# Kernel optimization log

Measured on AMD Instinct MI355X. Metric: run time of the kernel, lower is better.

Reference implementation:

```python
import jax, jax.numpy as jnp
import numpy as np
import math

B, S, D, H = 2, 2048, 1024, 16
HD = D // H  # head_dim = 64


def setup_inputs() -> dict:
    key = jax.random.key(0)
    k1, k2, k3, k4, k5 = jax.random.split(key, 5)
    scale_in = 1.0 / math.sqrt(D)
    return {
        "x": jax.random.normal(k1, (B, S, D), dtype=jnp.float32),
        "Wqkv": jax.random.normal(k2, (3 * D, D), dtype=jnp.float32) * scale_in,
        "bqkv": jax.random.normal(k3, (3 * D,), dtype=jnp.float32) * 0.01,
        "Wout": jax.random.normal(k4, (D, D), dtype=jnp.float32) * scale_in,
        "bout": jax.random.normal(k5, (D,), dtype=jnp.float32) * 0.01,
    }


def reference(x, Wqkv, bqkv, Wout, bout):
    Bs, Sl, Dm = x.shape
    # qkv projection: torch Linear is x @ W.T + b
    qkv = x @ Wqkv.T + bqkv                        # [B,S,3D]
    qkv = qkv.reshape(Bs, Sl, 3, H, HD)
    q, k, v = qkv[:, :, 0], qkv[:, :, 1], qkv[:, :, 2]  # each [B,S,H,d]
    softmax_scale = 1.0 / math.sqrt(HD)
    # NOTE: source einsum 'bshd,btjd->bsht' sums k over its head axis j.
    # Equivalent efficient form: pre-sum k (and v) over heads.
    k_sum = k.sum(axis=2)                          # [B,S,d]
    v_sum = v.sum(axis=2)                          # [B,S,d]
    scores = jnp.einsum('bshd,btd->bsht', q, k_sum) * softmax_scale  # [B,S,H,T]
    causal_mask = jnp.triu(jnp.ones((Sl, Sl), dtype=bool), k=1)      # [S,T]
    scores = jnp.where(causal_mask[None, :, None, :], -jnp.inf, scores)
    attn = jax.nn.softmax(scores, axis=-1)
    # dropout p=0.0 / eval mode -> identity
    out = jnp.einsum('bsht,btd->bshd', attn, v_sum)  # [B,S,H,d]
    out = out.reshape(Bs, Sl, Dm)
    return out @ Wout.T + bout
```

## Files before the change

kernel.cpp:

```cpp
#include <hip/hip_runtime.h>


#define S_LEN 2048
#define DIM 1024

using floatx4 = __attribute__((ext_vector_type(4))) float;
using halfx8  = __attribute__((ext_vector_type(8))) _Float16;
using halfx4  = __attribute__((ext_vector_type(4))) _Float16;

__device__ __forceinline__ floatx4 mfma16(halfx8 a, halfx8 b, floatx4 c) {
  return __builtin_amdgcn_mfma_f32_16x16x32_f16(a, b, c, 0, 0, 0);
}

__device__ __forceinline__ void gll16(const void* g, void* l) {
  __builtin_amdgcn_global_load_lds(
      (const __attribute__((address_space(1))) void*)g,
      (__attribute__((address_space(3))) void*)l, 16, 0, 0);
}

__global__ __launch_bounds__(256) void prep_all(
    const float* __restrict__ x, const float* __restrict__ wqkv,
    const float* __restrict__ bqkv, const float* __restrict__ wout,
    _Float16* __restrict__ xb, _Float16* __restrict__ wcomb,
    _Float16* __restrict__ woutb, float* __restrict__ bcomb) {
  int bx = blockIdx.x;
  if (bx < 6144) {
    size_t i4 = ((size_t)bx * 256 + threadIdx.x) * 4;
    const float* src;
    _Float16* dst;
    size_t off;
    if (i4 < 4194304) { src = x; dst = xb; off = i4; }
    else if (i4 < 5242880) { src = wqkv; dst = wcomb; off = i4 - 4194304; }
    else { src = wout; dst = woutb; off = i4 - 5242880; }
    float4 v = *(const float4*)(src + off);
    halfx4 o;
    o[0] = (_Float16)v.x; o[1] = (_Float16)v.y;
    o[2] = (_Float16)v.z; o[3] = (_Float16)v.w;
    *(halfx4*)(dst + off) = o;
  } else {
    int gid = (bx - 6144) * 256 + threadIdx.x;
    int c = gid >> 10, j = gid & 1023;
    int row0 = (c < 64) ? (1024 + c) : (2048 + c - 64);
    float s = 0.f;
#pragma unroll
    for (int h = 0; h < 16; ++h) s += wqkv[(size_t)(row0 + h * 64) * 1024 + j];
    wcomb[(size_t)1024 * 1024 + gid] = (_Float16)s;
    if (gid < 1024) bcomb[gid] = bqkv[gid];
    if (gid < 128) {
      int b0 = (gid < 64) ? (1024 + gid) : (2048 + gid - 64);
      float sb = 0.f;
#pragma unroll
      for (int h = 0; h < 16; ++h) sb += bqkv[b0 + h * 64];
      bcomb[1024 + gid] = sb;
    }
  }
}

template <int MODE>
__global__ __launch_bounds__(256, 2) void gemm_big(
    const _Float16* __restrict__ A, const _Float16* __restrict__ W,
    const float* __restrict__ bias, void* __restrict__ Cv,
    _Float16* __restrict__ kbo, _Float16* __restrict__ vto) {
  const int K = 1024;
  __shared__ _Float16 As[2][64][64];
  int tid = threadIdx.x;
  int lane = tid & 63, w = tid >> 6, ln = lane & 15, q4 = lane >> 4;
  int m0 = blockIdx.x * 64, n0 = blockIdx.y * 128;
  int rA = lane >> 3;
  int gA = ((lane & 7) ^ rA) * 8;
  const _Float16* agp = A + (size_t)(m0 + 16 * w + rA) * K + gA;
  const _Float16* wfp = W + (size_t)(n0 + w * 32 + ln) * K + q4 * 8;
  floatx4 acc[4][2] = {};
  halfx8 bf[2][2], bfn[2][2];
  gll16(agp, &As[0][16 * w][0]);
  gll16(agp + (size_t)8 * K, &As[0][16 * w + 8][0]);
#pragma unroll
  for (int ni = 0; ni < 2; ++ni)
#pragma unroll
    for (int kh = 0; kh < 2; ++kh)
      bf[ni][kh] = *(const halfx8*)(wfp + (size_t)ni * 16 * K + kh * 32);
  __syncthreads();
  for (int kt = 0; kt < K; kt += 64) {
    int cur = (kt >> 6) & 1;
    if (kt + 64 < K) {
      gll16(agp + kt + 64, &As[cur ^ 1][16 * w][0]);
      gll16(agp + (size_t)8 * K + kt + 64, &As[cur ^ 1][16 * w + 8][0]);
#pragma unroll
      for (int ni = 0; ni < 2; ++ni)
#pragma unroll
        for (int kh = 0; kh < 2; ++kh)
          bfn[ni][kh] =
              *(const halfx8*)(wfp + (size_t)ni * 16 * K + kt + 64 + kh * 32);
    }
#pragma unroll
    for (int kh = 0; kh < 2; ++kh) {
      int sw = ((q4 + 4 * kh) ^ (ln & 7)) * 8;
#pragma unroll
      for (int mi = 0; mi < 4; ++mi) {
        halfx8 af = *(const halfx8*)&As[cur][mi * 16 + ln][sw];
#pragma unroll
        for (int ni = 0; ni < 2; ++ni)
          acc[mi][ni] = mfma16(af, bf[ni][kh], acc[mi][ni]);
      }
    }
    if (kt + 64 < K) {
#pragma unroll
      for (int ni = 0; ni < 2; ++ni)
#pragma unroll
        for (int kh = 0; kh < 2; ++kh) bf[ni][kh] = bfn[ni][kh];
    }
    __syncthreads();
  }
  const float qscale = 0.18033688011112042f;
#pragma unroll
  for (int ni = 0; ni < 2; ++ni) {
    int col = n0 + w * 32 + ni * 16 + ln;
    float bv = bias[col];
    if constexpr (MODE == 1) {
#pragma unroll
      for (int mi = 0; mi < 4; ++mi)
#pragma unroll
        for (int i = 0; i < 4; ++i) {
          int row = m0 + mi * 16 + q4 * 4 + i;
          ((float*)Cv)[(size_t)row * 1024 + col] = acc[mi][ni][i] + bv;
        }
    } else {
      if (col < 1024) {
#pragma unroll
        for (int mi = 0; mi < 4; ++mi)
#pragma unroll
          for (int i = 0; i < 4; ++i) {
            int row = m0 + mi * 16 + q4 * 4 + i;
            ((_Float16*)Cv)[(size_t)row * 1024 + col] =
                (_Float16)((acc[mi][ni][i] + bv) * qscale);
          }
      } else if (col < 1088) {
        int ck = col - 1024;
#pragma unroll
        for (int mi = 0; mi < 4; ++mi)
#pragma unroll
          for (int i = 0; i < 4; ++i) {
            int row = m0 + mi * 16 + q4 * 4 + i;
            kbo[(size_t)row * 64 + ck] = (_Float16)(acc[mi][ni][i] + bv);
          }
      } else {
        int d = col - 1088;
#pragma unroll
        for (int mi = 0; mi < 4; ++mi) {
          int row0 = m0 + mi * 16 + q4 * 4;
          int bb = row0 >> 11, sps = row0 & 2047;
          halfx4 o;
#pragma unroll
          for (int i = 0; i < 4; ++i) o[i] = (_Float16)(acc[mi][ni][i] + bv);
          *(halfx4*)&vto[((size_t)((bb << 6) + d)) * S_LEN + sps] = o;
        }
      }
    }
  }
}

__global__ __launch_bounds__(256, 4) void flash_attn5(
    const _Float16* __restrict__ Qb, const _Float16* __restrict__ kb,
    const _Float16* __restrict__ vtb, _Float16* __restrict__ aob) {
  __shared__ _Float16 Ks[64][64];
  __shared__ _Float16 Vt[64][64];
  __shared__ _Float16 Ps[4][16][72];
  int tid = threadIdx.x;
  int lane = tid & 63, w = tid >> 6, ln = lane & 15, q4 = lane >> 4;
  int idx = 1023 - (int)blockIdx.x;
  int c = idx >> 1, b = idx & 1;
  int s0 = c * 4;
  int s = s0 + w;
  size_t bS = (size_t)b * S_LEN;

  const _Float16* qp = Qb + (bS + s) * DIM + ln * 64 + q4 * 8;
  halfx8 bq0 = *(const halfx8*)qp, bq1 = *(const halfx8*)(qp + 32);

  float m_run = -1e30f, l_run = 0.f;
  floatx4 oacc[4] = {};
  int rr = lane >> 3, gg = (lane & 7) ^ rr;
  const _Float16* kgp = kb + (bS + w * 16 + rr) * 64 + gg * 8;
  const _Float16* vgp = vtb + ((size_t)b * 64 + w * 16 + rr) * S_LEN + gg * 8;
  int swk0 = (q4 ^ (ln & 7)) * 8;
  int swk1 = ((q4 + 4) ^ (ln & 7)) * 8;
  _Float16* Pw = &Ps[w][0][0];
  int nt = (s0 >> 6) + 1;

  for (int it = 0; it < nt; ++it) {
    int t0 = it << 6;
    __syncthreads();
    gll16(kgp + (size_t)t0 * 64,        &Ks[w * 16][0]);
    gll16(kgp + (size_t)t0 * 64 + 512,  &Ks[w * 16 + 8][0]);
    gll16(vgp + t0,                     &Vt[w * 16][0]);
    gll16(vgp + t0 + (size_t)8 * S_LEN, &Vt[w * 16 + 8][0]);
    __syncthreads();

    floatx4 sf[4];
#pragma unroll
    for (int tf = 0; tf < 4; ++tf) {
      halfx8 ak0 = *(const halfx8*)&Ks[tf * 16 + ln][swk0];
      halfx8 ak1 = *(const halfx8*)&Ks[tf * 16 + ln][swk1];
      floatx4 z = {};
      z = mfma16(ak0, bq0, z);
      sf[tf] = mfma16(ak1, bq1, z);
    }
    if (it == nt - 1) {
#pragma unroll
      for (int tf = 0; tf < 4; ++tf)
#pragma unroll
        for (int i = 0; i < 4; ++i) {
          int t = t0 + tf * 16 + q4 * 4 + i;
          if (t > s) sf[tf][i] = -1e30f;
        }
    }
    float tm = fmaxf(fmaxf(sf[0][0], sf[0][1]), fmaxf(sf[0][2], sf[0][3]));
#pragma unroll
    for (int tf = 1; tf < 4; ++tf)
      tm = fmaxf(tm, fmaxf(fmaxf(sf[tf][0], sf[tf][1]),
                           fmaxf(sf[tf][2], sf[tf][3])));
    tm = fmaxf(tm, __shfl_xor(tm, 16));
    tm = fmaxf(tm, __shfl_xor(tm, 32));
    float mn = fmaxf(m_run, tm);
    float alpha = exp2f(m_run - mn);
    m_run = mn;
    float rs = 0.f;
#pragma unroll
    for (int tf = 0; tf < 4; ++tf) {
      float p0 = exp2f(sf[tf][0] - mn), p1 = exp2f(sf[tf][1] - mn);
      float p2 = exp2f(sf[tf][2] - mn), p3 = exp2f(sf[tf][3] - mn);
      rs += (p0 + p1) + (p2 + p3);
      halfx4 pk;
      pk[0] = (_Float16)p0; pk[1] = (_Float16)p1;
      pk[2] = (_Float16)p2; pk[3] = (_Float16)p3;
      *(halfx4*)&Pw[ln * 72 + tf * 16 + q4 * 4] = pk;
    }
    rs += __shfl_xor(rs, 16);
    rs += __shfl_xor(rs, 32);
    l_run = l_run * alpha + rs;
    halfx8 bp0 = *(const halfx8*)&Pw[ln * 72 + q4 * 8];
    halfx8 bp1 = *(const halfx8*)&Pw[ln * 72 + 32 + q4 * 8];
#pragma unroll
    for (int n2 = 0; n2 < 4; ++n2) {
      halfx8 av0 = *(const halfx8*)&Vt[n2 * 16 + ln][swk0];
      halfx8 av1 = *(const halfx8*)&Vt[n2 * 16 + ln][swk1];
#pragma unroll
      for (int i = 0; i < 4; ++i) oacc[n2][i] *= alpha;
      oacc[n2] = mfma16(av0, bp0, oacc[n2]);
      oacc[n2] = mfma16(av1, bp1, oacc[n2]);
    }
  }
  float inv = 1.0f / l_run;
#pragma unroll
  for (int n2 = 0; n2 < 4; ++n2) {
    halfx4 o;
#pragma unroll
    for (int i = 0; i < 4; ++i) o[i] = (_Float16)(oacc[n2][i] * inv);
    *(halfx4*)(aob + (bS + s) * DIM + ln * 64 + n2 * 16 + q4 * 4) = o;
  }
}

extern "C" void kernel_launch(void* const* d_in, const int* in_sizes, int n_in,
                              void* d_out, int out_size, void* d_ws,
                              size_t ws_size, hipStream_t stream) {
  const float* x    = (const float*)d_in[0];
  const float* wqkv = (const float*)d_in[1];
  const float* bqkv = (const float*)d_in[2];
  const float* wout = (const float*)d_in[3];
  const float* bout = (const float*)d_in[4];
  float* out = (float*)d_out;
  char* ws = (char*)d_ws;
  _Float16* xb    = (_Float16*)(ws);
  _Float16* qb    = (_Float16*)(ws + (8u << 20));
  _Float16* aob   = (_Float16*)(ws + (16u << 20));
  _Float16* kb    = (_Float16*)(ws + (24u << 20));
  _Float16* vtb   = (_Float16*)(ws + (24u << 20) + (512u << 10));
  _Float16* wcomb = (_Float16*)(ws + (25u << 20));
  _Float16* woutb = (_Float16*)(ws + (27u << 20) + (512u << 10));
  float*    bcomb = (float*)(ws + (29u << 20) + (512u << 10));

  hipLaunchKernelGGL(prep_all, dim3(6656), dim3(256), 0, stream,
                     x, wqkv, bqkv, wout, xb, wcomb, woutb, bcomb);
  hipLaunchKernelGGL((gemm_big<0>), dim3(64, 9), dim3(256), 0, stream,
                     xb, wcomb, bcomb, (void*)qb, kb, vtb);
  hipLaunchKernelGGL(flash_attn5, dim3(1024), dim3(256), 0, stream,
                     qb, kb, vtb, aob);
  hipLaunchKernelGGL((gemm_big<1>), dim3(64, 8), dim3(256), 0, stream,
                     aob, woutb, bout, (void*)out, nullptr, nullptr);
}
```

Baseline: 180.9 us.

## Use 32x32 MFMA in attention with register P exchange and stage W in LDS

The attention kernel moves from 16x16x32 to 32x32x16 MFMA with 128-thread blocks, each wave handling two query rows. The P matrix is passed between lanes in registers through cross-half shuffles instead of a trip through LDS. Rescaling of the accumulator and row sum is skipped when no lane's running max increased. In the GEMM, the weight tiles are now double-buffered in LDS through async global-to-LDS loads instead of direct global register prefetch. This raises LDS use and changes occupancy for both kernels.

```diff
diff --git a/kernel.cpp b/kernel.cpp
--- a/kernel.cpp
+++ b/kernel.cpp
@@ -4,12 +4,16 @@
 #define S_LEN 2048
 #define DIM 1024
 
-using floatx4 = __attribute__((ext_vector_type(4))) float;
-using halfx8  = __attribute__((ext_vector_type(8))) _Float16;
-using halfx4  = __attribute__((ext_vector_type(4))) _Float16;
+using floatx4  = __attribute__((ext_vector_type(4))) float;
+using floatx16 = __attribute__((ext_vector_type(16))) float;
+using halfx8   = __attribute__((ext_vector_type(8))) _Float16;
+using halfx4   = __attribute__((ext_vector_type(4))) _Float16;
 
 __device__ __forceinline__ floatx4 mfma16(halfx8 a, halfx8 b, floatx4 c) {
   return __builtin_amdgcn_mfma_f32_16x16x32_f16(a, b, c, 0, 0, 0);
+}
+__device__ __forceinline__ floatx16 mfma32(halfx8 a, halfx8 b, floatx16 c) {
+  return __builtin_amdgcn_mfma_f32_32x32x16_f16(a, b, c, 0, 0, 0);
 }
 
 __device__ __forceinline__ void gll16(const void* g, void* l) {
@@ -63,22 +67,19 @@
     _Float16* __restrict__ kbo, _Float16* __restrict__ vto) {
   const int K = 1024;
   __shared__ _Float16 As[2][64][64];
+  __shared__ _Float16 Ws[2][128][64];
   int tid = threadIdx.x;
   int lane = tid & 63, w = tid >> 6, ln = lane & 15, q4 = lane >> 4;
   int m0 = blockIdx.x * 64, n0 = blockIdx.y * 128;
-  int rA = lane >> 3;
-  int gA = ((lane & 7) ^ rA) * 8;
-  const _Float16* agp = A + (size_t)(m0 + 16 * w + rA) * K + gA;
-  const _Float16* wfp = W + (size_t)(n0 + w * 32 + ln) * K + q4 * 8;
+  int rr = lane >> 3, gg = ((lane & 7) ^ rr) * 8;
+  const _Float16* agp = A + (size_t)(m0 + 16 * w + rr) * K + gg;
+  const _Float16* wgp = W + (size_t)(n0 + 32 * w + rr) * K + gg;
   floatx4 acc[4][2] = {};
-  halfx8 bf[2][2], bfn[2][2];
   gll16(agp, &As[0][16 * w][0]);
   gll16(agp + (size_t)8 * K, &As[0][16 * w + 8][0]);
 #pragma unroll
-  for (int ni = 0; ni < 2; ++ni)
-#pragma unroll
-    for (int kh = 0; kh < 2; ++kh)
-      bf[ni][kh] = *(const halfx8*)(wfp + (size_t)ni * 16 * K + kh * 32);
+  for (int j = 0; j < 4; ++j)
+    gll16(wgp + (size_t)(8 * j) * K, &Ws[0][32 * w + 8 * j][0]);
   __syncthreads();
   for (int kt = 0; kt < K; kt += 64) {
     int cur = (kt >> 6) & 1;
@@ -86,28 +87,24 @@
       gll16(agp + kt + 64, &As[cur ^ 1][16 * w][0]);
       gll16(agp + (size_t)8 * K + kt + 64, &As[cur ^ 1][16 * w + 8][0]);
 #pragma unroll
-      for (int ni = 0; ni < 2; ++ni)
-#pragma unroll
-        for (int kh = 0; kh < 2; ++kh)
-          bfn[ni][kh] =
-              *(const halfx8*)(wfp + (size_t)ni * 16 * K + kt + 64 + kh * 32);
+      for (int j = 0; j < 4; ++j)
+        gll16(wgp + (size_t)(8 * j) * K + kt + 64,
+              &Ws[cur ^ 1][32 * w + 8 * j][0]);
     }
 #pragma unroll
     for (int kh = 0; kh < 2; ++kh) {
       int sw = ((q4 + 4 * kh) ^ (ln & 7)) * 8;
+      halfx8 bf[2];
+#pragma unroll
+      for (int ni = 0; ni < 2; ++ni)
+        bf[ni] = *(const halfx8*)&Ws[cur][w * 32 + ni * 16 + ln][sw];
 #pragma unroll
       for (int mi = 0; mi < 4; ++mi) {
         halfx8 af = *(const halfx8*)&As[cur][mi * 16 + ln][sw];
 #pragma unroll
         for (int ni = 0; ni < 2; ++ni)
-          acc[mi][ni] = mfma16(af, bf[ni][kh], acc[mi][ni]);
-      }
-    }
-    if (kt + 64 < K) {
-#pragma unroll
-      for (int ni = 0; ni < 2; ++ni)
-#pragma unroll
-        for (int kh = 0; kh < 2; ++kh) bf[ni][kh] = bfn[ni][kh];
+          acc[mi][ni] = mfma16(af, bf[ni], acc[mi][ni]);
+      }
     }
     __syncthreads();
   }
@@ -159,104 +156,133 @@
   }
 }
 
-__global__ __launch_bounds__(256, 4) void flash_attn5(
+__global__ __launch_bounds__(128, 2) void flash_attn6(
     const _Float16* __restrict__ Qb, const _Float16* __restrict__ kb,
     const _Float16* __restrict__ vtb, _Float16* __restrict__ aob) {
   __shared__ _Float16 Ks[64][64];
   __shared__ _Float16 Vt[64][64];
-  __shared__ _Float16 Ps[4][16][72];
   int tid = threadIdx.x;
-  int lane = tid & 63, w = tid >> 6, ln = lane & 15, q4 = lane >> 4;
+  int lane = tid & 63, w = tid >> 6;
+  int col = lane & 31, hk = lane >> 5;
+  int h = lane & 15, si = (lane >> 4) & 1;
   int idx = 1023 - (int)blockIdx.x;
   int c = idx >> 1, b = idx & 1;
   int s0 = c * 4;
-  int s = s0 + w;
+  int s = s0 + 2 * w + si;
   size_t bS = (size_t)b * S_LEN;
 
-  const _Float16* qp = Qb + (bS + s) * DIM + ln * 64 + q4 * 8;
-  halfx8 bq0 = *(const halfx8*)qp, bq1 = *(const halfx8*)(qp + 32);
-
+  halfx8 bq[4];
+  {
+    const _Float16* qp = Qb + (bS + s) * DIM + h * 64 + hk * 8;
+#pragma unroll
+    for (int kd = 0; kd < 4; ++kd) bq[kd] = *(const halfx8*)(qp + kd * 16);
+  }
   float m_run = -1e30f, l_run = 0.f;
-  floatx4 oacc[4] = {};
-  int rr = lane >> 3, gg = (lane & 7) ^ rr;
-  const _Float16* kgp = kb + (bS + w * 16 + rr) * 64 + gg * 8;
-  const _Float16* vgp = vtb + ((size_t)b * 64 + w * 16 + rr) * S_LEN + gg * 8;
-  int swk0 = (q4 ^ (ln & 7)) * 8;
-  int swk1 = ((q4 + 4) ^ (ln & 7)) * 8;
-  _Float16* Pw = &Ps[w][0][0];
+  floatx16 oacc[2] = {};
+  int rr = lane >> 3, gg8 = ((lane & 7) ^ rr) * 8;
+  const _Float16* kgp = kb + (bS + w * 32 + rr) * 64 + gg8;
+  const _Float16* vgp = vtb + ((size_t)b * 64 + w * 32 + rr) * S_LEN + gg8;
+  int swb = col & 7;
   int nt = (s0 >> 6) + 1;
 
   for (int it = 0; it < nt; ++it) {
     int t0 = it << 6;
     __syncthreads();
-    gll16(kgp + (size_t)t0 * 64,        &Ks[w * 16][0]);
-    gll16(kgp + (size_t)t0 * 64 + 512,  &Ks[w * 16 + 8][0]);
-    gll16(vgp + t0,                     &Vt[w * 16][0]);
-    gll16(vgp + t0 + (size_t)8 * S_LEN, &Vt[w * 16 + 8][0]);
+#pragma unroll
+    for (int j = 0; j < 4; ++j) {
+      gll16(kgp + (size_t)(t0 + 8 * j) * 64, &Ks[w * 32 + 8 * j][0]);
+      gll16(vgp + (size_t)(8 * j) * S_LEN + t0, &Vt[w * 32 + 8 * j][0]);
+    }
     __syncthreads();
 
-    floatx4 sf[4];
-#pragma unroll
-    for (int tf = 0; tf < 4; ++tf) {
-      halfx8 ak0 = *(const halfx8*)&Ks[tf * 16 + ln][swk0];
-      halfx8 ak1 = *(const halfx8*)&Ks[tf * 16 + ln][swk1];
-      floatx4 z = {};
-      z = mfma16(ak0, bq0, z);
-      sf[tf] = mfma16(ak1, bq1, z);
+    floatx16 sf[2];
+#pragma unroll
+    for (int tt = 0; tt < 2; ++tt) {
+      floatx16 z = {};
+#pragma unroll
+      for (int kd = 0; kd < 4; ++kd) {
+        halfx8 ak =
+            *(const halfx8*)&Ks[tt * 32 + col][((kd * 2 + hk) ^ swb) * 8];
+        z = mfma32(ak, bq[kd], z);
+      }
+      sf[tt] = z;
     }
     if (it == nt - 1) {
-#pragma unroll
-      for (int tf = 0; tf < 4; ++tf)
-#pragma unroll
-        for (int i = 0; i < 4; ++i) {
-          int t = t0 + tf * 16 + q4 * 4 + i;
-          if (t > s) sf[tf][i] = -1e30f;
+      int base = s - t0 - 4 * hk;
+#pragma unroll
+      for (int tt = 0; tt < 2; ++tt)
+#pragma unroll
+        for (int r = 0; r < 16; ++r) {
+          int cr = (r & 3) + 8 * (r >> 2) + 32 * tt;
+          if (cr > base) sf[tt][r] = -1e30f;
         }
     }
-    float tm = fmaxf(fmaxf(sf[0][0], sf[0][1]), fmaxf(sf[0][2], sf[0][3]));
-#pragma unroll
-    for (int tf = 1; tf < 4; ++tf)
-      tm = fmaxf(tm, fmaxf(fmaxf(sf[tf][0], sf[tf][1]),
-                           fmaxf(sf[tf][2], sf[tf][3])));
-    tm = fmaxf(tm, __shfl_xor(tm, 16));
+    float tm = sf[0][0];
+#pragma unroll
+    for (int tt = 0; tt < 2; ++tt)
+#pragma unroll
+      for (int r = 0; r < 16; ++r) tm = fmaxf(tm, sf[tt][r]);
     tm = fmaxf(tm, __shfl_xor(tm, 32));
-    float mn = fmaxf(m_run, tm);
-    float alpha = exp2f(m_run - mn);
+    float mo = m_run;
+    float mn = fmaxf(mo, tm);
     m_run = mn;
+    if (__any(tm > mo)) {
+      float alpha = exp2f(mo - mn);
+#pragma unroll
+      for (int dd = 0; dd < 2; ++dd)
+#pragma unroll
+        for (int r = 0; r < 16; ++r) oacc[dd][r] *= alpha;
+      l_run *= alpha;
+    }
     float rs = 0.f;
-#pragma unroll
-    for (int tf = 0; tf < 4; ++tf) {
-      float p0 = exp2f(sf[tf][0] - mn), p1 = exp2f(sf[tf][1] - mn);
-      float p2 = exp2f(sf[tf][2] - mn), p3 = exp2f(sf[tf][3] - mn);
-      rs += (p0 + p1) + (p2 + p3);
-      halfx4 pk;
-      pk[0] = (_Float16)p0; pk[1] = (_Float16)p1;
-      pk[2] = (_Float16)p2; pk[3] = (_Float16)p3;
-      *(halfx4*)&Pw[ln * 72 + tf * 16 + q4 * 4] = pk;
-    }
-    rs += __shfl_xor(rs, 16);
+    int pk[16];
+#pragma unroll
+    for (int tt = 0; tt < 2; ++tt)
+#pragma unroll
+      for (int i = 0; i < 8; ++i) {
+        float p0 = exp2f(sf[tt][2 * i] - mn);
+        float p1 = exp2f(sf[tt][2 * i + 1] - mn);
+        rs += p0 + p1;
+        union { _Float16 hh[2]; int ii; } u;
+        u.hh[0] = (_Float16)p0;
+        u.hh[1] = (_Float16)p1;
+        pk[tt * 8 + i] = u.ii;
+      }
     rs += __shfl_xor(rs, 32);
-    l_run = l_run * alpha + rs;
-    halfx8 bp0 = *(const halfx8*)&Pw[ln * 72 + q4 * 8];
-    halfx8 bp1 = *(const halfx8*)&Pw[ln * 72 + 32 + q4 * 8];
-#pragma unroll
-    for (int n2 = 0; n2 < 4; ++n2) {
-      halfx8 av0 = *(const halfx8*)&Vt[n2 * 16 + ln][swk0];
-      halfx8 av1 = *(const halfx8*)&Vt[n2 * 16 + ln][swk1];
-#pragma unroll
-      for (int i = 0; i < 4; ++i) oacc[n2][i] *= alpha;
-      oacc[n2] = mfma16(av0, bp0, oacc[n2]);
-      oacc[n2] = mfma16(av1, bp1, oacc[n2]);
+    l_run += rs;
+#pragma unroll
+    for (int kt = 0; kt < 4; ++kt) {
+      int tt = kt >> 1, q0 = 2 * (kt & 1), q1 = q0 + 1;
+      int own0 = hk ? pk[tt * 8 + 2 * q1]     : pk[tt * 8 + 2 * q0];
+      int own1 = hk ? pk[tt * 8 + 2 * q1 + 1] : pk[tt * 8 + 2 * q0 + 1];
+      int snd0 = hk ? pk[tt * 8 + 2 * q0]     : pk[tt * 8 + 2 * q1];
+      int snd1 = hk ? pk[tt * 8 + 2 * q0 + 1] : pk[tt * 8 + 2 * q1 + 1];
+      int rcv0 = __shfl_xor(snd0, 32);
+      int rcv1 = __shfl_xor(snd1, 32);
+      union { int ii[4]; halfx8 hh; } u;
+      u.ii[0] = hk ? rcv0 : own0;
+      u.ii[1] = hk ? rcv1 : own1;
+      u.ii[2] = hk ? own0 : rcv0;
+      u.ii[3] = hk ? own1 : rcv1;
+#pragma unroll
+      for (int dd = 0; dd < 2; ++dd) {
+        halfx8 av =
+            *(const halfx8*)&Vt[dd * 32 + col][((kt * 2 + hk) ^ swb) * 8];
+        oacc[dd] = mfma32(av, u.hh, oacc[dd]);
+      }
     }
   }
   float inv = 1.0f / l_run;
 #pragma unroll
-  for (int n2 = 0; n2 < 4; ++n2) {
-    halfx4 o;
-#pragma unroll
-    for (int i = 0; i < 4; ++i) o[i] = (_Float16)(oacc[n2][i] * inv);
-    *(halfx4*)(aob + (bS + s) * DIM + ln * 64 + n2 * 16 + q4 * 4) = o;
-  }
+  for (int dd = 0; dd < 2; ++dd)
+#pragma unroll
+    for (int rg = 0; rg < 4; ++rg) {
+      halfx4 o;
+#pragma unroll
+      for (int i2 = 0; i2 < 4; ++i2)
+        o[i2] = (_Float16)(oacc[dd][rg * 4 + i2] * inv);
+      *(halfx4*)(aob + (bS + s) * DIM + h * 64 + dd * 32 + rg * 8 + hk * 4) = o;
+    }
 }
 
 extern "C" void kernel_launch(void* const* d_in, const int* in_sizes, int n_in,
@@ -282,7 +308,7 @@
                      x, wqkv, bqkv, wout, xb, wcomb, woutb, bcomb);
   hipLaunchKernelGGL((gemm_big<0>), dim3(64, 9), dim3(256), 0, stream,
                      xb, wcomb, bcomb, (void*)qb, kb, vtb);
-  hipLaunchKernelGGL(flash_attn5, dim3(1024), dim3(256), 0, stream,
+  hipLaunchKernelGGL(flash_attn6, dim3(1024), dim3(128), 0, stream,
                      qb, kb, vtb, aob);
   hipLaunchKernelGGL((gemm_big<1>), dim3(64, 8), dim3(256), 0, stream,
                      aob, woutb, bout, (void*)out, nullptr, nullptr);
```

Result: slower. 186.0 us (+2.8%).

## Enlarge GEMM tiles to 128x128 with LDS-staged weights and double attention KV tile

Applied to the files above, without the earlier changes.

The projection GEMMs switch from 64x128 tiles, where weights are loaded straight from global into registers, to 128x128 tiles. Both A and W are staged in LDS, and each wave computes a 64x64 sub-tile, which raises reuse per load and halves the grid. The attention kernel now loads 128 keys and values per iteration instead of 64 and processes them as two 64-wide sub-steps, halving the number of barrier-separated load phases. The cost is that the GEMM loses its software double-buffering, leaving loads unoverlapped and using fewer blocks, and causal rows may load keys they never use.

```diff
diff --git a/kernel.cpp b/kernel.cpp
--- a/kernel.cpp
+++ b/kernel.cpp
@@ -57,101 +57,86 @@
 }
 
 template <int MODE>
-__global__ __launch_bounds__(256, 2) void gemm_big(
+__global__ __launch_bounds__(256, 2) void gemm_t2(
     const _Float16* __restrict__ A, const _Float16* __restrict__ W,
     const float* __restrict__ bias, void* __restrict__ Cv,
     _Float16* __restrict__ kbo, _Float16* __restrict__ vto) {
   const int K = 1024;
-  __shared__ _Float16 As[2][64][64];
+  __shared__ _Float16 As[128][64];
+  __shared__ _Float16 Ws[128][64];
   int tid = threadIdx.x;
   int lane = tid & 63, w = tid >> 6, ln = lane & 15, q4 = lane >> 4;
-  int m0 = blockIdx.x * 64, n0 = blockIdx.y * 128;
-  int rA = lane >> 3;
-  int gA = ((lane & 7) ^ rA) * 8;
-  const _Float16* agp = A + (size_t)(m0 + 16 * w + rA) * K + gA;
-  const _Float16* wfp = W + (size_t)(n0 + w * 32 + ln) * K + q4 * 8;
-  floatx4 acc[4][2] = {};
-  halfx8 bf[2][2], bfn[2][2];
-  gll16(agp, &As[0][16 * w][0]);
-  gll16(agp + (size_t)8 * K, &As[0][16 * w + 8][0]);
-#pragma unroll
-  for (int ni = 0; ni < 2; ++ni)
-#pragma unroll
-    for (int kh = 0; kh < 2; ++kh)
-      bf[ni][kh] = *(const halfx8*)(wfp + (size_t)ni * 16 * K + kh * 32);
-  __syncthreads();
+  int m0 = blockIdx.x * 128, n0 = blockIdx.y * 128;
+  int mh = (w & 1) * 64, nh = (w >> 1) * 64;
+  int rr = lane >> 3, gg = ((lane & 7) ^ rr) * 8;
+  const _Float16* agp = A + (size_t)(m0 + w * 32 + rr) * K + gg;
+  const _Float16* wgp = W + (size_t)(n0 + w * 32 + rr) * K + gg;
+  floatx4 acc[4][4] = {};
   for (int kt = 0; kt < K; kt += 64) {
-    int cur = (kt >> 6) & 1;
-    if (kt + 64 < K) {
-      gll16(agp + kt + 64, &As[cur ^ 1][16 * w][0]);
-      gll16(agp + (size_t)8 * K + kt + 64, &As[cur ^ 1][16 * w + 8][0]);
-#pragma unroll
-      for (int ni = 0; ni < 2; ++ni)
-#pragma unroll
-        for (int kh = 0; kh < 2; ++kh)
-          bfn[ni][kh] =
-              *(const halfx8*)(wfp + (size_t)ni * 16 * K + kt + 64 + kh * 32);
-    }
+    __syncthreads();
+#pragma unroll
+    for (int j = 0; j < 4; ++j) {
+      gll16(agp + (size_t)(8 * j) * K + kt, &As[w * 32 + 8 * j][0]);
+      gll16(wgp + (size_t)(8 * j) * K + kt, &Ws[w * 32 + 8 * j][0]);
+    }
+    __syncthreads();
 #pragma unroll
     for (int kh = 0; kh < 2; ++kh) {
       int sw = ((q4 + 4 * kh) ^ (ln & 7)) * 8;
-#pragma unroll
-      for (int mi = 0; mi < 4; ++mi) {
-        halfx8 af = *(const halfx8*)&As[cur][mi * 16 + ln][sw];
-#pragma unroll
-        for (int ni = 0; ni < 2; ++ni)
-          acc[mi][ni] = mfma16(af, bf[ni][kh], acc[mi][ni]);
-      }
-    }
-    if (kt + 64 < K) {
-#pragma unroll
-      for (int ni = 0; ni < 2; ++ni)
-#pragma unroll
-        for (int kh = 0; kh < 2; ++kh) bf[ni][kh] = bfn[ni][kh];
-    }
-    __syncthreads();
+      halfx8 bf[4];
+#pragma unroll
+      for (int nf = 0; nf < 4; ++nf)
+        bf[nf] = *(const halfx8*)&Ws[nh + nf * 16 + ln][sw];
+#pragma unroll
+      for (int mf = 0; mf < 4; ++mf) {
+        halfx8 af = *(const halfx8*)&As[mh + mf * 16 + ln][sw];
+#pragma unroll
+        for (int nf = 0; nf < 4; ++nf)
+          acc[mf][nf] = mfma16(af, bf[nf], acc[mf][nf]);
+      }
+    }
   }
   const float qscale = 0.18033688011112042f;
 #pragma unroll
-  for (int ni = 0; ni < 2; ++ni) {
-    int col = n0 + w * 32 + ni * 16 + ln;
+  for (int nf = 0; nf < 4; ++nf) {
+    int col = n0 + nh + nf * 16 + ln;
     float bv = bias[col];
     if constexpr (MODE == 1) {
 #pragma unroll
-      for (int mi = 0; mi < 4; ++mi)
+      for (int mf = 0; mf < 4; ++mf)
 #pragma unroll
         for (int i = 0; i < 4; ++i) {
-          int row = m0 + mi * 16 + q4 * 4 + i;
-          ((float*)Cv)[(size_t)row * 1024 + col] = acc[mi][ni][i] + bv;
+          int row = m0 + mh + mf * 16 + q4 * 4 + i;
+          ((float*)Cv)[(size_t)row * 1024 + col] = acc[mf][nf][i] + bv;
         }
     } else {
       if (col < 1024) {
 #pragma unroll
-        for (int mi = 0; mi < 4; ++mi)
+        for (int mf = 0; mf < 4; ++mf)
 #pragma unroll
           for (int i = 0; i < 4; ++i) {
-            int row = m0 + mi * 16 + q4 * 4 + i;
+            int row = m0 + mh + mf * 16 + q4 * 4 + i;
             ((_Float16*)Cv)[(size_t)row * 1024 + col] =
-                (_Float16)((acc[mi][ni][i] + bv) * qscale);
+                (_Float16)((acc[mf][nf][i] + bv) * qscale);
           }
       } else if (col < 1088) {
         int ck = col - 1024;
 #pragma unroll
-        for (int mi = 0; mi < 4; ++mi)
+        for (int mf = 0; mf < 4; ++mf)
 #pragma unroll
           for (int i = 0; i < 4; ++i) {
-            int row = m0 + mi * 16 + q4 * 4 + i;
-            kbo[(size_t)row * 64 + ck] = (_Float16)(acc[mi][ni][i] + bv);
+            int row = m0 + mh + mf * 16 + q4 * 4 + i;
+            kbo[(size_t)row * 64 + ck] = (_Float16)(acc[mf][nf][i] + bv);
           }
       } else {
         int d = col - 1088;
 #pragma unroll
-        for (int mi = 0; mi < 4; ++mi) {
-          int row0 = m0 + mi * 16 + q4 * 4;
+        for (int mf = 0; mf < 4; ++mf) {
+          int row0 = m0 + mh + mf * 16 + q4 * 4;
           int bb = row0 >> 11, sps = row0 & 2047;
           halfx4 o;
 #pragma unroll
-          for (int i = 0; i < 4; ++i) o[i] = (_Float16)(acc[mi][ni][i] + bv);
+          for (int i = 0; i < 4; ++i) o[i] = (_Float16)(acc[mf][nf][i] + bv);
           *(halfx4*)&vto[((size_t)((bb << 6) + d)) * S_LEN + sps] = o;
         }
       }
@@ -159,11 +144,11 @@
   }
 }
 
-__global__ __launch_bounds__(256, 4) void flash_attn5(
+__global__ __launch_bounds__(256, 4) void flash_attn7(
     const _Float16* __restrict__ Qb, const _Float16* __restrict__ kb,
     const _Float16* __restrict__ vtb, _Float16* __restrict__ aob) {
-  __shared__ _Float16 Ks[64][64];
-  __shared__ _Float16 Vt[64][64];
+  __shared__ _Float16 Ks[128][64];
+  __shared__ _Float16 Vt[64][128];
   __shared__ _Float16 Ps[4][16][72];
   int tid = threadIdx.x;
   int lane = tid & 63, w = tid >> 6, ln = lane & 15, q4 = lane >> 4;
@@ -178,75 +163,90 @@
 
   float m_run = -1e30f, l_run = 0.f;
   floatx4 oacc[4] = {};
-  int rr = lane >> 3, gg = (lane & 7) ^ rr;
-  const _Float16* kgp = kb + (bS + w * 16 + rr) * 64 + gg * 8;
-  const _Float16* vgp = vtb + ((size_t)b * 64 + w * 16 + rr) * S_LEN + gg * 8;
+
+  int rr = lane >> 3, ggk = ((lane & 7) ^ rr) * 8;
+  const _Float16* kgp = kb + (bS + w * 32 + rr) * 64 + ggk;
+  int vrow = (lane >> 4);
+  int vhalf = (lane >> 3) & 1, vg = lane & 7;
+  const _Float16* vgp[4];
+#pragma unroll
+  for (int j = 0; j < 4; ++j) {
+    int row = w * 16 + 4 * j + vrow;
+    vgp[j] = vtb + ((size_t)b * 64 + row) * S_LEN + vhalf * 64 +
+             ((vg ^ (row & 7)) * 8);
+  }
   int swk0 = (q4 ^ (ln & 7)) * 8;
   int swk1 = ((q4 + 4) ^ (ln & 7)) * 8;
   _Float16* Pw = &Ps[w][0][0];
-  int nt = (s0 >> 6) + 1;
+  int nt = (s0 >> 7) + 1;
 
   for (int it = 0; it < nt; ++it) {
-    int t0 = it << 6;
-    __syncthreads();
-    gll16(kgp + (size_t)t0 * 64,        &Ks[w * 16][0]);
-    gll16(kgp + (size_t)t0 * 64 + 512,  &Ks[w * 16 + 8][0]);
-    gll16(vgp + t0,                     &Vt[w * 16][0]);
-    gll16(vgp + t0 + (size_t)8 * S_LEN, &Vt[w * 16 + 8][0]);
-    __syncthreads();
-
-    floatx4 sf[4];
-#pragma unroll
-    for (int tf = 0; tf < 4; ++tf) {
-      halfx8 ak0 = *(const halfx8*)&Ks[tf * 16 + ln][swk0];
-      halfx8 ak1 = *(const halfx8*)&Ks[tf * 16 + ln][swk1];
-      floatx4 z = {};
-      z = mfma16(ak0, bq0, z);
-      sf[tf] = mfma16(ak1, bq1, z);
-    }
-    if (it == nt - 1) {
-#pragma unroll
-      for (int tf = 0; tf < 4; ++tf)
-#pragma unroll
-        for (int i = 0; i < 4; ++i) {
-          int t = t0 + tf * 16 + q4 * 4 + i;
-          if (t > s) sf[tf][i] = -1e30f;
-        }
-    }
-    float tm = fmaxf(fmaxf(sf[0][0], sf[0][1]), fmaxf(sf[0][2], sf[0][3]));
-#pragma unroll
-    for (int tf = 1; tf < 4; ++tf)
-      tm = fmaxf(tm, fmaxf(fmaxf(sf[tf][0], sf[tf][1]),
-                           fmaxf(sf[tf][2], sf[tf][3])));
-    tm = fmaxf(tm, __shfl_xor(tm, 16));
-    tm = fmaxf(tm, __shfl_xor(tm, 32));
-    float mn = fmaxf(m_run, tm);
-    float alpha = exp2f(m_run - mn);
-    m_run = mn;
-    float rs = 0.f;
-#pragma unroll
-    for (int tf = 0; tf < 4; ++tf) {
-      float p0 = exp2f(sf[tf][0] - mn), p1 = exp2f(sf[tf][1] - mn);
-      float p2 = exp2f(sf[tf][2] - mn), p3 = exp2f(sf[tf][3] - mn);
-      rs += (p0 + p1) + (p2 + p3);
-      halfx4 pk;
-      pk[0] = (_Float16)p0; pk[1] = (_Float16)p1;
-      pk[2] = (_Float16)p2; pk[3] = (_Float16)p3;
-      *(halfx4*)&Pw[ln * 72 + tf * 16 + q4 * 4] = pk;
-    }
-    rs += __shfl_xor(rs, 16);
-    rs += __shfl_xor(rs, 32);
-    l_run = l_run * alpha + rs;
-    halfx8 bp0 = *(const halfx8*)&Pw[ln * 72 + q4 * 8];
-    halfx8 bp1 = *(const halfx8*)&Pw[ln * 72 + 32 + q4 * 8];
-#pragma unroll
-    for (int n2 = 0; n2 < 4; ++n2) {
-      halfx8 av0 = *(const halfx8*)&Vt[n2 * 16 + ln][swk0];
-      halfx8 av1 = *(const halfx8*)&Vt[n2 * 16 + ln][swk1];
-#pragma unroll
-      for (int i = 0; i < 4; ++i) oacc[n2][i] *= alpha;
-      oacc[n2] = mfma16(av0, bp0, oacc[n2]);
-      oacc[n2] = mfma16(av1, bp1, oacc[n2]);
+    int t0 = it << 7;
+    __syncthreads();
+#pragma unroll
+    for (int j = 0; j < 4; ++j) {
+      gll16(kgp + (size_t)(t0 + 8 * j) * 64, &Ks[w * 32 + 8 * j][0]);
+      gll16(vgp[j] + t0, &Vt[w * 16 + 4 * j][0]);
+    }
+    __syncthreads();
+
+#pragma unroll
+    for (int tq = 0; tq < 2; ++tq) {
+      int t0q = t0 + tq * 64;
+      if (t0q > s) break;
+      floatx4 sf[4];
+#pragma unroll
+      for (int tf = 0; tf < 4; ++tf) {
+        halfx8 ak0 = *(const halfx8*)&Ks[tq * 64 + tf * 16 + ln][swk0];
+        halfx8 ak1 = *(const halfx8*)&Ks[tq * 64 + tf * 16 + ln][swk1];
+        floatx4 z = {};
+        z = mfma16(ak0, bq0, z);
+        sf[tf] = mfma16(ak1, bq1, z);
+      }
+      if (t0q + 63 > s) {
+#pragma unroll
+        for (int tf = 0; tf < 4; ++tf)
+#pragma unroll
+          for (int i = 0; i < 4; ++i) {
+            int t = t0q + tf * 16 + q4 * 4 + i;
+            if (t > s) sf[tf][i] = -1e30f;
+          }
+      }
+      float tm = fmaxf(fmaxf(sf[0][0], sf[0][1]), fmaxf(sf[0][2], sf[0][3]));
+#pragma unroll
+      for (int tf = 1; tf < 4; ++tf)
+        tm = fmaxf(tm, fmaxf(fmaxf(sf[tf][0], sf[tf][1]),
+                             fmaxf(sf[tf][2], sf[tf][3])));
+      tm = fmaxf(tm, __shfl_xor(tm, 16));
+      tm = fmaxf(tm, __shfl_xor(tm, 32));
+      float mn = fmaxf(m_run, tm);
+      float alpha = exp2f(m_run - mn);
+      m_run = mn;
+      float rs = 0.f;
+#pragma unroll
+      for (int tf = 0; tf < 4; ++tf) {
+        float p0 = exp2f(sf[tf][0] - mn), p1 = exp2f(sf[tf][1] - mn);
+        float p2 = exp2f(sf[tf][2] - mn), p3 = exp2f(sf[tf][3] - mn);
+        rs += (p0 + p1) + (p2 + p3);
+        halfx4 pk;
+        pk[0] = (_Float16)p0; pk[1] = (_Float16)p1;
+        pk[2] = (_Float16)p2; pk[3] = (_Float16)p3;
+        *(halfx4*)&Pw[ln * 72 + tf * 16 + q4 * 4] = pk;
+      }
+      rs += __shfl_xor(rs, 16);
+      rs += __shfl_xor(rs, 32);
+      l_run = l_run * alpha + rs;
+      halfx8 bp0 = *(const halfx8*)&Pw[ln * 72 + q4 * 8];
+      halfx8 bp1 = *(const halfx8*)&Pw[ln * 72 + 32 + q4 * 8];
+#pragma unroll
+      for (int n2 = 0; n2 < 4; ++n2) {
+        halfx8 av0 = *(const halfx8*)&Vt[n2 * 16 + ln][tq * 64 + swk0];
+        halfx8 av1 = *(const halfx8*)&Vt[n2 * 16 + ln][tq * 64 + swk1];
+#pragma unroll
+        for (int i = 0; i < 4; ++i) oacc[n2][i] *= alpha;
+        oacc[n2] = mfma16(av0, bp0, oacc[n2]);
+        oacc[n2] = mfma16(av1, bp1, oacc[n2]);
+      }
     }
   }
   float inv = 1.0f / l_run;
@@ -280,10 +280,10 @@
 
   hipLaunchKernelGGL(prep_all, dim3(6656), dim3(256), 0, stream,
                      x, wqkv, bqkv, wout, xb, wcomb, woutb, bcomb);
-  hipLaunchKernelGGL((gemm_big<0>), dim3(64, 9), dim3(256), 0, stream,
+  hipLaunchKernelGGL((gemm_t2<0>), dim3(32, 9), dim3(256), 0, stream,
                      xb, wcomb, bcomb, (void*)qb, kb, vtb);
-  hipLaunchKernelGGL(flash_attn5, dim3(1024), dim3(256), 0, stream,
+  hipLaunchKernelGGL(flash_attn7, dim3(1024), dim3(256), 0, stream,
                      qb, kb, vtb, aob);
-  hipLaunchKernelGGL((gemm_big<1>), dim3(64, 8), dim3(256), 0, stream,
+  hipLaunchKernelGGL((gemm_t2<1>), dim3(32, 8), dim3(256), 0, stream,
                      aob, woutb, bout, (void*)out, nullptr, nullptr);
 }
```

New measurement: 169.4 us. 1.07x faster.
